# Optimization experiments

Measured on AMD Instinct MI355X. Metric: run time of the kernel, lower is better.

Reference implementation:

```python
import jax, jax.numpy as jnp
import numpy as np

T = 32
TAU = 2.0
ALPHA = 2.0
V_TH = 1.0
V_RESET = 0.0
PHI = 0.05
MAX_ACTION = 1.0
STATE_DIM, ACTION_DIM = 376, 17
H1, H2 = 400, 300
BATCH = 8192


@jax.custom_vjp
def spike_fn(x):
    # Heaviside with ATan surrogate gradient (spikingjelly surrogate.ATan)
    return (x >= 0.0).astype(x.dtype)

def _spike_fwd(x):
    return spike_fn(x), x

def _spike_bwd(x, g):
    return (g * (ALPHA / 2.0) / (1.0 + (jnp.pi / 2.0 * ALPHA * x) ** 2),)

spike_fn.defvjp(_spike_fwd, _spike_bwd)


def setup_inputs() -> dict:
    key = jax.random.key(0)
    ks = jax.random.split(key, 8)
    d_in = STATE_DIM + ACTION_DIM
    s = lambda k, shape, fan: jax.random.uniform(k, shape, jnp.float32, -1.0, 1.0) / np.sqrt(fan)
    return {
        "state": jax.random.normal(ks[0], (BATCH, STATE_DIM), jnp.float32),
        "action": jax.random.normal(ks[1], (BATCH, ACTION_DIM), jnp.float32),
        "W1": s(ks[2], (d_in, H1), d_in), "b1": s(ks[3], (H1,), d_in),
        "W2": s(ks[4], (H1, H2), H1),   "b2": s(ks[5], (H2,), H1),
        "W3": s(ks[6], (H2, ACTION_DIM), H2), "b3": s(ks[7], (ACTION_DIM,), H2),
    }


def reference(state, action, W1, b1, W2, b2, W3, b3):
    # input repeated over T -> layer-1 pre-activation current is step-invariant
    inp = jnp.concatenate([state, action], axis=1)          # [B, state+action]
    x1 = inp @ W1 + b1                                      # [B, H1]
    B = state.shape[0]

    def step(carry, _):
        v1, v2, v3 = carry
        # LIF layer 1: charge v += (x - (v - v_reset))/tau, fire, hard reset
        v1 = v1 + (x1 - (v1 - V_RESET)) / TAU
        s1 = spike_fn(v1 - V_TH)
        v1 = s1 * V_RESET + (1.0 - s1) * v1
        # LIF layer 2
        x2 = s1 @ W2 + b2
        v2 = v2 + (x2 - (v2 - V_RESET)) / TAU
        s2 = spike_fn(v2 - V_TH)
        v2 = s2 * V_RESET + (1.0 - s2) * v2
        # non-spiking LIF layer 3: charge only, output membrane potential
        x3 = s2 @ W3 + b3
        v3 = v3 + (x3 - (v3 - V_RESET)) / TAU
        return (v1, v2, v3), v3

    init = (jnp.full((B, H1), V_RESET, x1.dtype),
            jnp.full((B, H2), V_RESET, x1.dtype),
            jnp.full((B, ACTION_DIM), V_RESET, x1.dtype))
    _, v3_seq = jax.lax.scan(step, init, None, length=T)    # [T, B, action_dim]
    a = v3_seq.max(axis=0)
    a = PHI * MAX_ACTION * jnp.tanh(a)
    return jnp.clip(a + action, -MAX_ACTION, MAX_ACTION)
```

## Files before the change

### kernel.cpp

```cpp
#include <hip/hip_runtime.h>
#include <math.h>

#define SDIM 376
#define ADIM 17
#define DIN  393
#define H1   400
#define H2   300
#define TSTEPS 32
#define KP 416
#define NKT 13

typedef __bf16 bf16x8 __attribute__((ext_vector_type(8)));
typedef float  f32x4  __attribute__((ext_vector_type(4)));


__global__ __launch_bounds__(256) void prep_fused(
    const float* __restrict__ state, const float* __restrict__ action,
    const float* __restrict__ W1,
    __bf16* __restrict__ A_sw, __bf16* __restrict__ B_sw,
    int B, int npack) {
    const int bid = blockIdx.x, tid = threadIdx.x;
    if (bid < npack) {
        int idx = bid * 256 + tid;
        int r = idx / 52, c = idx - r * 52;
        if (r >= B) return;
        int g0 = c * 8;
        float v[8];
        if (g0 + 7 < SDIM) {
            float4 a = *(const float4*)&state[r * SDIM + g0];
            float4 b = *(const float4*)&state[r * SDIM + g0 + 4];
            v[0]=a.x; v[1]=a.y; v[2]=a.z; v[3]=a.w; v[4]=b.x; v[5]=b.y; v[6]=b.z; v[7]=b.w;
        } else {
            #pragma unroll
            for (int e = 0; e < 8; ++e) {
                int k = g0 + e;
                v[e] = (k < SDIM) ? state[r * SDIM + k]
                     : (k < DIN)  ? action[r * ADIM + k - SDIM] : 0.f;
            }
        }
        bf16x8 o;
        #pragma unroll
        for (int e = 0; e < 8; ++e) o[e] = (__bf16)v[e];
        int kt = g0 >> 5, quad = (g0 >> 3) & 3;
        *(bf16x8*)&A_sw[(((size_t)(r >> 4) * NKT + kt) * 64 + (quad << 4) + (r & 15)) * 8] = o;
    } else {
        int idx = (bid - npack) * 256 + tid;
        if (idx >= H1 * KP) return;
        int k = idx / H1, n = idx - k * H1;
        float val = (k < DIN) ? W1[k * H1 + n] : 0.f;
        int ntile = n >> 4, kt = k >> 5, quad = (k >> 3) & 3;
        B_sw[(((size_t)ntile * NKT + kt) * 64 + (quad << 4) + (n & 15)) * 8 + (k & 7)] = (__bf16)val;
    }
}

__global__ __launch_bounds__(256) void gemm_mask(
    const __bf16* __restrict__ A_sw, const __bf16* __restrict__ B_sw,
    const float* __restrict__ b1, unsigned short* __restrict__ maskbuf) {
    const int tid = threadIdx.x, wave = tid >> 6, lane = tid & 63;
    const int quad = lane >> 4, l16 = lane & 15;
    const int mtile = blockIdx.x * 4 + wave;
    const int bn0 = blockIdx.y * 80;

    f32x4 acc[5];
    #pragma unroll
    for (int n = 0; n < 5; ++n) acc[n] = (f32x4){0.f, 0.f, 0.f, 0.f};

    const __bf16* ap = A_sw + ((size_t)mtile * NKT * 64 + lane) * 8;
    const __bf16* bp = B_sw + ((size_t)(blockIdx.y * 5) * NKT * 64 + lane) * 8;

    #pragma unroll
    for (int kt = 0; kt < NKT; ++kt) {
        bf16x8 af = *(const bf16x8*)(ap + (size_t)kt * 512);
        #pragma unroll
        for (int n = 0; n < 5; ++n) {
            bf16x8 bfrag = *(const bf16x8*)(bp + ((size_t)n * NKT + kt) * 512);
            acc[n] = __builtin_amdgcn_mfma_f32_16x16x32_bf16(af, bfrag, acc[n], 0, 0, 0);
        }
    }

    float b1v[5];
    #pragma unroll
    for (int n = 0; n < 5; ++n) b1v[n] = b1[bn0 + n * 16 + l16];
    const int cbase = bn0 >> 4;
    const int bm0 = mtile * 16;
    #pragma unroll
    for (int n = 0; n < 5; ++n)
        #pragma unroll
        for (int reg = 0; reg < 4; ++reg) {
            unsigned long long bal = __ballot(acc[n][reg] + b1v[n] >= 0.99f);
            if (l16 == 0)
                maskbuf[(size_t)(bm0 + quad * 4 + reg) * 32 + cbase + n] =
                    (unsigned short)(bal >> (quad * 16));
        }
}

__global__ __launch_bounds__(256) void snn_actor(
    const unsigned long long* __restrict__ mask64,
    const float* __restrict__ state, const float* __restrict__ action,
    const float* __restrict__ W1, const float* __restrict__ b1,
    const float* __restrict__ W2, const float* __restrict__ b2,
    const float* __restrict__ W3, const float* __restrict__ b3,
    float* __restrict__ out) {
    const int lane = threadIdx.x & 63;
    const int row  = blockIdx.x * 4 + (threadIdx.x >> 6);

    unsigned long long mw = 0;
    if (lane < 7) {
        mw = mask64[row * 8 + lane];
        if (lane == 6) mw &= 0xFFFFULL;
    }

    const float act = (lane < ADIM) ? action[row * ADIM + lane] : 0.f;
    const float b3v = (lane < ADIM) ? b3[lane] : 0.f;

    float gv;
    {
        float v3 = 0.f, vm = -3.0e38f;
        #pragma unroll
        for (int t = 0; t < TSTEPS; ++t) { v3 += (b3v - v3) * 0.5f; vm = fmaxf(vm, v3); }
        gv = 0.05f * tanhf(vm);
    }

    float bound[5];
    #pragma unroll
    for (int c = 0; c < 5; ++c) { int j = lane + 64 * c; bound[c] = (j < H2) ? b2[j] : 0.f; }
    #pragma unroll 1
    for (int w = 0; w < 7; ++w) {
        unsigned long long m = __shfl(mw, w);
        while (m) {
            int b0 = __builtin_ctzll(m); m &= m - 1;
            const float* r0 = W2 + (w * 64 + b0) * H2;
            if (m) {
                int b1i = __builtin_ctzll(m); m &= m - 1;
                const float* r1 = W2 + (w * 64 + b1i) * H2;
                float t0[5], t1[5];
                #pragma unroll
                for (int c = 0; c < 5; ++c) {
                    int j = lane + 64 * c;
                    t0[c] = (j < H2) ? r0[j] : 0.f;
                    t1[c] = (j < H2) ? r1[j] : 0.f;
                }
                #pragma unroll
                for (int c = 0; c < 5; ++c)
                    bound[c] += fmaxf(t0[c], 0.f) + fmaxf(t1[c], 0.f);
            } else {
                #pragma unroll
                for (int c = 0; c < 5; ++c) {
                    int j = lane + 64 * c;
                    bound[c] += (j < H2) ? fmaxf(r0[j], 0.f) : 0.f;
                }
            }
        }
    }
    bool ok = true;
    #pragma unroll
    for (int c = 0; c < 5; ++c) ok = ok && (bound[c] < 0.999f);
    if (__all(ok)) {
        if (lane < ADIM) out[row * ADIM + lane] = fminf(fmaxf(gv + act, -1.f), 1.f);
        return;
    }

    float x1v[7];
    #pragma unroll
    for (int s = 0; s < 7; ++s) { int col = lane + 64 * s; x1v[s] = (col < H1) ? b1[col] : 0.f; }
    for (int k = 0; k < DIN; ++k) {
        float ik = (k < SDIM) ? state[row * SDIM + k] : action[row * ADIM + k - SDIM];
        #pragma unroll
        for (int s = 0; s < 7; ++s) {
            int col = lane + 64 * s;
            if (col < H1) x1v[s] += ik * W1[k * H1 + col];
        }
    }
    float b2v[5];
    #pragma unroll
    for (int c = 0; c < 5; ++c) { int j = lane + 64 * c; b2v[c] = (j < H2) ? b2[j] : 0.f; }
    float v1[7], v2[5], v3 = 0.f, vmax = -3.0e38f;
    #pragma unroll
    for (int s = 0; s < 7; ++s) v1[s] = 0.f;
    #pragma unroll
    for (int c = 0; c < 5; ++c) v2[c] = 0.f;
    for (int t = 0; t < TSTEPS; ++t) {
        float x2[5];
        #pragma unroll
        for (int c = 0; c < 5; ++c) x2[c] = b2v[c];
        #pragma unroll
        for (int s = 0; s < 7; ++s) {
            float v = v1[s] + (x1v[s] - v1[s]) * 0.5f;
            bool sp = v >= 1.0f;
            v1[s] = sp ? 0.f : v;
            unsigned long long m = __ballot(sp);
            while (m) {
                int j = __builtin_ctzll(m); m &= m - 1;
                const float* wr = W2 + (s * 64 + j) * H2;
                #pragma unroll
                for (int c = 0; c < 5; ++c) {
                    int col = lane + 64 * c;
                    if (col < H2) x2[c] += wr[col];
                }
            }
        }
        float x3 = b3v;
        #pragma unroll
        for (int c = 0; c < 5; ++c) {
            float v = v2[c] + (x2[c] - v2[c]) * 0.5f;
            int col = lane + 64 * c;
            bool sp = (col < H2) && (v >= 1.0f);
            v2[c] = sp ? 0.f : v;
            unsigned long long m = __ballot(sp);
            while (m) {
                int j = __builtin_ctzll(m); m &= m - 1;
                if (lane < ADIM) x3 += W3[(c * 64 + j) * ADIM + lane];
            }
        }
        v3 += (x3 - v3) * 0.5f;
        vmax = fmaxf(vmax, v3);
    }
    if (lane < ADIM)
        out[row * ADIM + lane] = fminf(fmaxf(0.05f * tanhf(vmax) + act, -1.f), 1.f);
}

extern "C" void kernel_launch(void* const* d_in, const int* in_sizes, int n_in,
                              void* d_out, int out_size, void* d_ws, size_t ws_size,
                              hipStream_t stream) {
    const float* state  = (const float*)d_in[0];
    const float* action = (const float*)d_in[1];
    const float* W1     = (const float*)d_in[2];
    const float* b1     = (const float*)d_in[3];
    const float* W2     = (const float*)d_in[4];
    const float* b2     = (const float*)d_in[5];
    const float* W3     = (const float*)d_in[6];
    const float* b3     = (const float*)d_in[7];
    float* out = (float*)d_out;

    const int B = in_sizes[0] / SDIM;

    char* p = (char*)d_ws;
    __bf16* A_sw = (__bf16*)p;                 p += (size_t)B * KP * 2;
    __bf16* B_sw = (__bf16*)p;                 p += (size_t)H1 * KP * 2;
    unsigned short* maskbuf = (unsigned short*)p;
    unsigned long long* mask64 = (unsigned long long*)p;

    const int npack = (B * 52 + 255) / 256;
    const int nw1t  = (H1 * KP + 255) / 256;
    prep_fused<<<npack + nw1t, 256, 0, stream>>>(state, action, W1, A_sw, B_sw, B, npack);
    gemm_mask<<<dim3(B / 64, 5), 256, 0, stream>>>(A_sw, B_sw, b1, maskbuf);
    snn_actor<<<B / 4, 256, 0, stream>>>(mask64, state, action,
                                         W1, b1, W2, b2, W3, b3, out);
}
```

Baseline: 104.4 us.

## Fuse prep, GEMM and SNN kernels into one cooperative persistent kernel

Merges the three launches (bf16 packing, layer-1 GEMM with spike-mask ballot, per-row SNN) into a single cooperative kernel with grid-wide syncs between phases. Each phase runs as grid-stride loops over its original block units. This removes two kernel launch gaps and inter-kernel drain/fill. The costs are the grid.sync barriers, register pressure from inlining all phases into one kernel (which can lower occupancy), and host-side occupancy queries on every call. The old three-kernel path stays as a fallback.

```diff
diff --git a/kernel.cpp b/kernel.cpp
--- a/kernel.cpp
+++ b/kernel.cpp
@@ -1,5 +1,8 @@
 #include <hip/hip_runtime.h>
+#include <hip/hip_cooperative_groups.h>
 #include <math.h>
+
+namespace cg = cooperative_groups;
 
 #define SDIM 376
 #define ADIM 17
@@ -14,12 +17,10 @@
 typedef float  f32x4  __attribute__((ext_vector_type(4)));
 
 
-__global__ __launch_bounds__(256) void prep_fused(
-    const float* __restrict__ state, const float* __restrict__ action,
-    const float* __restrict__ W1,
-    __bf16* __restrict__ A_sw, __bf16* __restrict__ B_sw,
+__device__ __forceinline__ void phase_pack_unit(
+    int bid, int tid, const float* __restrict__ state, const float* __restrict__ action,
+    const float* __restrict__ W1, __bf16* __restrict__ A_sw, __bf16* __restrict__ B_sw,
     int B, int npack) {
-    const int bid = blockIdx.x, tid = threadIdx.x;
     if (bid < npack) {
         int idx = bid * 256 + tid;
         int r = idx / 52, c = idx - r * 52;
@@ -28,8 +29,8 @@
         float v[8];
         if (g0 + 7 < SDIM) {
             float4 a = *(const float4*)&state[r * SDIM + g0];
-            float4 b = *(const float4*)&state[r * SDIM + g0 + 4];
-            v[0]=a.x; v[1]=a.y; v[2]=a.z; v[3]=a.w; v[4]=b.x; v[5]=b.y; v[6]=b.z; v[7]=b.w;
+            float4 bb = *(const float4*)&state[r * SDIM + g0 + 4];
+            v[0]=a.x; v[1]=a.y; v[2]=a.z; v[3]=a.w; v[4]=bb.x; v[5]=bb.y; v[6]=bb.z; v[7]=bb.w;
         } else {
             #pragma unroll
             for (int e = 0; e < 8; ++e) {
@@ -53,20 +54,20 @@
     }
 }
 
-__global__ __launch_bounds__(256) void gemm_mask(
-    const __bf16* __restrict__ A_sw, const __bf16* __restrict__ B_sw,
+__device__ __forceinline__ void phase_gemm_unit(
+    int bx, int by, int tid, const __bf16* __restrict__ A_sw, const __bf16* __restrict__ B_sw,
     const float* __restrict__ b1, unsigned short* __restrict__ maskbuf) {
-    const int tid = threadIdx.x, wave = tid >> 6, lane = tid & 63;
+    const int wave = tid >> 6, lane = tid & 63;
     const int quad = lane >> 4, l16 = lane & 15;
-    const int mtile = blockIdx.x * 4 + wave;
-    const int bn0 = blockIdx.y * 80;
+    const int mtile = bx * 4 + wave;
+    const int bn0 = by * 80;
 
     f32x4 acc[5];
     #pragma unroll
     for (int n = 0; n < 5; ++n) acc[n] = (f32x4){0.f, 0.f, 0.f, 0.f};
 
     const __bf16* ap = A_sw + ((size_t)mtile * NKT * 64 + lane) * 8;
-    const __bf16* bp = B_sw + ((size_t)(blockIdx.y * 5) * NKT * 64 + lane) * 8;
+    const __bf16* bp = B_sw + ((size_t)(by * 5) * NKT * 64 + lane) * 8;
 
     #pragma unroll
     for (int kt = 0; kt < NKT; ++kt) {
@@ -77,11 +78,10 @@
             acc[n] = __builtin_amdgcn_mfma_f32_16x16x32_bf16(af, bfrag, acc[n], 0, 0, 0);
         }
     }
-
     float b1v[5];
     #pragma unroll
     for (int n = 0; n < 5; ++n) b1v[n] = b1[bn0 + n * 16 + l16];
-    const int cbase = bn0 >> 4;
+    const int cbase = by * 5;
     const int bm0 = mtile * 16;
     #pragma unroll
     for (int n = 0; n < 5; ++n)
@@ -94,32 +94,25 @@
         }
 }
 
-__global__ __launch_bounds__(256) void snn_actor(
-    const unsigned long long* __restrict__ mask64,
+__device__ __forceinline__ void phase_snn_row(
+    int row, int lane, const unsigned long long* __restrict__ mask64,
     const float* __restrict__ state, const float* __restrict__ action,
     const float* __restrict__ W1, const float* __restrict__ b1,
     const float* __restrict__ W2, const float* __restrict__ b2,
     const float* __restrict__ W3, const float* __restrict__ b3,
     float* __restrict__ out) {
-    const int lane = threadIdx.x & 63;
-    const int row  = blockIdx.x * 4 + (threadIdx.x >> 6);
-
     unsigned long long mw = 0;
     if (lane < 7) {
         mw = mask64[row * 8 + lane];
         if (lane == 6) mw &= 0xFFFFULL;
     }
-
     const float act = (lane < ADIM) ? action[row * ADIM + lane] : 0.f;
     const float b3v = (lane < ADIM) ? b3[lane] : 0.f;
 
-    float gv;
-    {
-        float v3 = 0.f, vm = -3.0e38f;
-        #pragma unroll
-        for (int t = 0; t < TSTEPS; ++t) { v3 += (b3v - v3) * 0.5f; vm = fmaxf(vm, v3); }
-        gv = 0.05f * tanhf(vm);
-    }
+    float v3c = 0.f, vmc = -3.0e38f;
+    #pragma unroll
+    for (int t = 0; t < TSTEPS; ++t) { v3c += (b3v - v3c) * 0.5f; vmc = fmaxf(vmc, v3c); }
+    const float gv = 0.05f * tanhf(vmc);
 
     float bound[5];
     #pragma unroll
@@ -128,11 +121,11 @@
     for (int w = 0; w < 7; ++w) {
         unsigned long long m = __shfl(mw, w);
         while (m) {
-            int b0 = __builtin_ctzll(m); m &= m - 1;
-            const float* r0 = W2 + (w * 64 + b0) * H2;
+            int c0 = __builtin_ctzll(m); m &= m - 1;
+            const float* r0 = W2 + (w * 64 + c0) * H2;
             if (m) {
-                int b1i = __builtin_ctzll(m); m &= m - 1;
-                const float* r1 = W2 + (w * 64 + b1i) * H2;
+                int c1 = __builtin_ctzll(m); m &= m - 1;
+                const float* r1 = W2 + (w * 64 + c1) * H2;
                 float t0[5], t1[5];
                 #pragma unroll
                 for (int c = 0; c < 5; ++c) {
@@ -141,8 +134,7 @@
                     t1[c] = (j < H2) ? r1[j] : 0.f;
                 }
                 #pragma unroll
-                for (int c = 0; c < 5; ++c)
-                    bound[c] += fmaxf(t0[c], 0.f) + fmaxf(t1[c], 0.f);
+                for (int c = 0; c < 5; ++c) bound[c] += fmaxf(t0[c], 0.f) + fmaxf(t1[c], 0.f);
             } else {
                 #pragma unroll
                 for (int c = 0; c < 5; ++c) {
@@ -152,10 +144,10 @@
             }
         }
     }
-    bool ok = true;
-    #pragma unroll
-    for (int c = 0; c < 5; ++c) ok = ok && (bound[c] < 0.999f);
-    if (__all(ok)) {
+    bool okb = true;
+    #pragma unroll
+    for (int c = 0; c < 5; ++c) okb = okb && (bound[c] < 0.999f);
+    if (__all(okb)) {
         if (lane < ADIM) out[row * ADIM + lane] = fminf(fmaxf(gv + act, -1.f), 1.f);
         return;
     }
@@ -219,6 +211,59 @@
         out[row * ADIM + lane] = fminf(fmaxf(0.05f * tanhf(vmax) + act, -1.f), 1.f);
 }
 
+__global__ __launch_bounds__(256) void actor_fused(
+    const float* __restrict__ state, const float* __restrict__ action,
+    const float* __restrict__ W1, const float* __restrict__ b1,
+    const float* __restrict__ W2, const float* __restrict__ b2,
+    const float* __restrict__ W3, const float* __restrict__ b3,
+    __bf16* __restrict__ A_sw, __bf16* __restrict__ B_sw,
+    unsigned short* __restrict__ maskbuf, float* __restrict__ out, int B) {
+    cg::grid_group grid = cg::this_grid();
+    const int tid = threadIdx.x;
+    const int nb = gridDim.x;
+    const int npack = (B * 52 + 255) / 256;
+    const int nw1t  = (H1 * KP + 255) / 256;
+
+    for (int bid = blockIdx.x; bid < npack + nw1t; bid += nb)
+        phase_pack_unit(bid, tid, state, action, W1, A_sw, B_sw, B, npack);
+    grid.sync();
+
+    const int nbx = B / 64;
+    for (int unit = blockIdx.x; unit < nbx * 5; unit += nb)
+        phase_gemm_unit(unit % nbx, unit / nbx, tid, A_sw, B_sw, b1, maskbuf);
+    grid.sync();
+
+    const unsigned long long* mask64 = (const unsigned long long*)maskbuf;
+    const int lane = tid & 63;
+    for (int unit = blockIdx.x; unit < B / 4; unit += nb)
+        phase_snn_row(unit * 4 + (tid >> 6), lane, mask64, state, action,
+                      W1, b1, W2, b2, W3, b3, out);
+}
+
+__global__ __launch_bounds__(256) void prep_k(
+    const float* __restrict__ state, const float* __restrict__ action,
+    const float* __restrict__ W1, __bf16* __restrict__ A_sw, __bf16* __restrict__ B_sw,
+    int B, int npack) {
+    phase_pack_unit(blockIdx.x, threadIdx.x, state, action, W1, A_sw, B_sw, B, npack);
+}
+
+__global__ __launch_bounds__(256) void gemm_k(
+    const __bf16* __restrict__ A_sw, const __bf16* __restrict__ B_sw,
+    const float* __restrict__ b1, unsigned short* __restrict__ maskbuf) {
+    phase_gemm_unit(blockIdx.x, blockIdx.y, threadIdx.x, A_sw, B_sw, b1, maskbuf);
+}
+
+__global__ __launch_bounds__(256) void snn_k(
+    const unsigned long long* __restrict__ mask64,
+    const float* __restrict__ state, const float* __restrict__ action,
+    const float* __restrict__ W1, const float* __restrict__ b1,
+    const float* __restrict__ W2, const float* __restrict__ b2,
+    const float* __restrict__ W3, const float* __restrict__ b3,
+    float* __restrict__ out) {
+    phase_snn_row(blockIdx.x * 4 + (threadIdx.x >> 6), threadIdx.x & 63, mask64,
+                  state, action, W1, b1, W2, b2, W3, b3, out);
+}
+
 extern "C" void kernel_launch(void* const* d_in, const int* in_sizes, int n_in,
                               void* d_out, int out_size, void* d_ws, size_t ws_size,
                               hipStream_t stream) {
@@ -232,18 +277,34 @@
     const float* b3     = (const float*)d_in[7];
     float* out = (float*)d_out;
 
-    const int B = in_sizes[0] / SDIM;
+    int B = in_sizes[0] / SDIM;
 
     char* p = (char*)d_ws;
     __bf16* A_sw = (__bf16*)p;                 p += (size_t)B * KP * 2;
     __bf16* B_sw = (__bf16*)p;                 p += (size_t)H1 * KP * 2;
     unsigned short* maskbuf = (unsigned short*)p;
-    unsigned long long* mask64 = (unsigned long long*)p;
-
     const int npack = (B * 52 + 255) / 256;
     const int nw1t  = (H1 * KP + 255) / 256;
-    prep_fused<<<npack + nw1t, 256, 0, stream>>>(state, action, W1, A_sw, B_sw, B, npack);
-    gemm_mask<<<dim3(B / 64, 5), 256, 0, stream>>>(A_sw, B_sw, b1, maskbuf);
-    snn_actor<<<B / 4, 256, 0, stream>>>(mask64, state, action,
-                                         W1, b1, W2, b2, W3, b3, out);
-}
+
+    int occ = 0;
+    hipError_t qe = hipOccupancyMaxActiveBlocksPerMultiprocessor(&occ, actor_fused, 256, 0);
+    int numCU = 256;
+    int dev = 0;
+    if (hipGetDevice(&dev) == hipSuccess)
+        hipDeviceGetAttribute(&numCU, hipDeviceAttributeMultiprocessorCount, dev);
+
+    bool coop_ok = (qe == hipSuccess) && (occ >= 1);
+    if (coop_ok) {
+        int grid = occ * numCU;
+        if (grid > 2048) grid = 2048;
+        void* kargs[] = {&state, &action, &W1, &b1, &W2, &b2, &W3, &b3,
+                         &A_sw, &B_sw, &maskbuf, &out, &B};
+        hipError_t le = hipLaunchCooperativeKernel((const void*)actor_fused, dim3(grid),
+                                                   dim3(256), kargs, 0, stream);
+        if (le == hipSuccess) return;
+    }
+    prep_k<<<npack + nw1t, 256, 0, stream>>>(state, action, W1, A_sw, B_sw, B, npack);
+    gemm_k<<<dim3(B / 64, 5), 256, 0, stream>>>(A_sw, B_sw, b1, maskbuf);
+    snn_k<<<B / 4, 256, 0, stream>>>((const unsigned long long*)maskbuf, state, action,
+                                     W1, b1, W2, b2, W3, b3, out);
+}
```

Result: slower. 263.9 us (+152.8%).
